# Kernel tuning notes

Hardware: AMD Instinct MI355X
Metric: run time of the kernel (lower is better)

## Reference

```python
import jax, jax.numpy as jnp
import numpy as np

T, BLOCK, SIG = 4096, 1024, 1024
LAM = 0.25


def _lstm_cell(x, h, c, Wih, Whh, bih, bhh):
    # PyTorch LSTM gate order: i, f, g, o
    gates = x @ Wih.T + h @ Whh.T + bih + bhh  # [1, 4H]
    i, f, g, o = jnp.split(gates, 4, axis=-1)
    i = jax.nn.sigmoid(i)
    f = jax.nn.sigmoid(f)
    g = jnp.tanh(g)
    o = jax.nn.sigmoid(o)
    c_new = f * c + i * g
    h_new = o * jnp.tanh(c_new)
    return h_new, c_new


def setup_inputs() -> dict:
    key = jax.random.key(0)
    ks = jax.random.split(key, 9)
    ke = 1.0 / np.sqrt(SIG)
    kd = 1.0 / np.sqrt(BLOCK)
    inputs = jax.random.normal(ks[0], (T, 1, BLOCK), dtype=jnp.float32)
    enc_Wih = jax.random.uniform(ks[1], (4 * SIG, BLOCK), jnp.float32, -ke, ke)
    enc_Whh = jax.random.uniform(ks[2], (4 * SIG, SIG), jnp.float32, -ke, ke)
    enc_bih = jax.random.uniform(ks[3], (4 * SIG,), jnp.float32, -ke, ke)
    enc_bhh = jax.random.uniform(ks[4], (4 * SIG,), jnp.float32, -ke, ke)
    dec_Wih = jax.random.uniform(ks[5], (4 * BLOCK, SIG), jnp.float32, -kd, kd)
    dec_Whh = jax.random.uniform(ks[6], (4 * BLOCK, BLOCK), jnp.float32, -kd, kd)
    dec_bih = jax.random.uniform(ks[7], (4 * BLOCK,), jnp.float32, -kd, kd)
    dec_bhh = jax.random.uniform(ks[8], (4 * BLOCK,), jnp.float32, -kd, kd)
    return {"inputs": inputs, "enc_Wih": enc_Wih, "enc_Whh": enc_Whh,
            "enc_bih": enc_bih, "enc_bhh": enc_bhh, "dec_Wih": dec_Wih,
            "dec_Whh": dec_Whh, "dec_bih": dec_bih, "dec_bhh": dec_bhh}


def reference(inputs, enc_Wih, enc_Whh, enc_bih, enc_bhh,
              dec_Wih, dec_Whh, dec_bih, dec_bhh):
    H = enc_Whh.shape[1]
    B = inputs.shape[-1]

    # encode: full-sequence LSTM, zero initial state, batch=1
    def enc_step(carry, x):
        h, c = carry
        h, c = _lstm_cell(x, h, c, enc_Wih, enc_Whh, enc_bih, enc_bhh)
        return (h, c), h

    h0 = jnp.zeros((1, H), inputs.dtype)
    c0 = jnp.zeros((1, H), inputs.dtype)
    _, signal = jax.lax.scan(enc_step, (h0, c0), inputs)  # [T, 1, H]

    # decode: one LSTM step per i; h0 reset to inputs[i], cell state carried
    def dec_step(c, xs):
        x, h_init = xs  # x = signal[i+1], h_init = inputs[i]
        h, c = _lstm_cell(x, h_init, c, dec_Wih, dec_Whh, dec_bih, dec_bhh)
        return c, h

    cdec0 = jnp.zeros((1, B), inputs.dtype)
    _, decoded = jax.lax.scan(dec_step, cdec0, (signal[1:], inputs[:-1]))  # [T-1, 1, B]

    target = inputs[1:]
    mse_loss = jnp.mean((decoded - target) ** 2)
    l1_reg = jnp.sum(jnp.abs(signal)) / signal.size
    loss = mse_loss + LAM * l1_reg
    return loss, mse_loss, l1_reg
```

## Files before the change

kernel.cpp:

```cpp
#include <hip/hip_runtime.h>
#include <math.h>

#define TSTEPS 4096
#define DIM 1024
#define GDIM 4096
#define ENC_NB 64
#define NSEG 64
#define SEGLEN 64

typedef short bf16x8 __attribute__((ext_vector_type(8)));
typedef float f32x4 __attribute__((ext_vector_type(4)));
typedef unsigned int uint4v __attribute__((ext_vector_type(4)));

__device__ __forceinline__ float sigmoidf_(float x) {
    return 1.0f / (1.0f + expf(-x));
}

__device__ __forceinline__ void loadcvt(const float* __restrict__ p,
                                        bf16x8& hi, bf16x8& lo)
{
    float4 a = *(const float4*)p;
    float4 b = *(const float4*)(p + 4);
    float f[8] = {a.x, a.y, a.z, a.w, b.x, b.y, b.z, b.w};
    uint4v hw, lw;
    #pragma unroll
    for (int j = 0; j < 4; ++j) {
        unsigned u0 = __float_as_uint(f[2*j]);
        unsigned u1 = __float_as_uint(f[2*j+1]);
        unsigned m0 = u0 & 0xffff0000u;
        unsigned m1 = u1 & 0xffff0000u;
        float r0 = f[2*j]   - __uint_as_float(m0);
        float r1 = f[2*j+1] - __uint_as_float(m1);
        hw[j] = __builtin_amdgcn_perm(u1, u0, 0x07060302u);
        lw[j] = __builtin_amdgcn_perm(__float_as_uint(r1), __float_as_uint(r0),
                                      0x07060302u);
    }
    hi = __builtin_bit_cast(bf16x8, hw);
    lo = __builtin_bit_cast(bf16x8, lw);
}

template<bool DUAL>
__global__ __launch_bounds__(256)
void gemm_split(const float* __restrict__ A1, const float* __restrict__ B1,
                const float* __restrict__ A2, const float* __restrict__ B2,
                const float* __restrict__ bias1, const float* __restrict__ bias2,
                float* __restrict__ C, int N)
{
    const int lane = threadIdx.x & 63;
    const int wid  = threadIdx.x >> 6;
    const int m0 = blockIdx.y * 128 + (wid >> 1) * 64;
    const int n0 = blockIdx.x * 128 + (wid & 1) * 64;
    const int rA   = m0 + (lane & 15);
    const int cB   = n0 + (lane & 15);
    const int koff = (lane >> 4) * 8;

    f32x4 acc[4][4] = {};

    const int npass = DUAL ? 2 : 1;
    for (int pass = 0; pass < npass; ++pass) {
        const float* __restrict__ A = (DUAL && pass) ? A2 : A1;
        const float* __restrict__ B = (DUAL && pass) ? B2 : B1;
        for (int k0 = 0; k0 < 1024; k0 += 32) {
            bf16x8 ah[4], al[4], bh[4], bl[4];
            #pragma unroll
            for (int i = 0; i < 4; ++i)
                loadcvt(A + (size_t)(rA + i * 16) * 1024 + k0 + koff, ah[i], al[i]);
            #pragma unroll
            for (int j = 0; j < 4; ++j)
                loadcvt(B + (size_t)(cB + j * 16) * 1024 + k0 + koff, bh[j], bl[j]);
            #pragma unroll
            for (int i = 0; i < 4; ++i)
                #pragma unroll
                for (int j = 0; j < 4; ++j) {
                    acc[i][j] = __builtin_amdgcn_mfma_f32_16x16x32_bf16(
                        ah[i], bh[j], acc[i][j], 0, 0, 0);
                    acc[i][j] = __builtin_amdgcn_mfma_f32_16x16x32_bf16(
                        ah[i], bl[j], acc[i][j], 0, 0, 0);
                    acc[i][j] = __builtin_amdgcn_mfma_f32_16x16x32_bf16(
                        al[i], bh[j], acc[i][j], 0, 0, 0);
                }
        }
    }

    const int er = (lane >> 4) * 4;
    const int ec = lane & 15;
    #pragma unroll
    for (int j = 0; j < 4; ++j) {
        int col = n0 + j * 16 + ec;
        float bb = bias1[col] + bias2[col];
        #pragma unroll
        for (int i = 0; i < 4; ++i) {
            int rowb = m0 + i * 16 + er;
            #pragma unroll
            for (int r = 0; r < 4; ++r)
                C[(size_t)(rowb + r) * N + col] = acc[i][j][r] + bb;
        }
    }
}

__global__ __launch_bounds__(1024)
void encoder_scan(const float* __restrict__ Xg,
                  const float* __restrict__ Whh,
                  float* __restrict__ signal,
                  unsigned long long* __restrict__ slots)
{
    const int b = blockIdx.x;
    const int t = threadIdx.x;
    const int hbase = b * 16;
    const int r = t >> 4, sub = t & 15;
    const int q = r >> 4, hi = r & 15;
    const int grow = q * 1024 + hbase + hi;

    float4 w[16];
    {
        const float4* wrow = (const float4*)(Whh + (size_t)grow * 1024 + sub * 64);
        #pragma unroll
        for (int i = 0; i < 16; ++i) w[i] = wrow[i];
    }

    __shared__ float hls[16 * 68];
    __shared__ float gl[4][16];
    __shared__ float cs[16];
    if (t < 16) cs[t] = 0.f;
    __syncthreads();

    for (int step = 0; step < TSTEPS; ++step) {
        float xg = 0.f;
        if (sub == 0) xg = Xg[(size_t)step * GDIM + grow];

        unsigned long long v;
        {
            const unsigned long long* sp = slots + (size_t)(step & 1) * 1024 + t;
            while (true) {
                v = __hip_atomic_load(sp, __ATOMIC_RELAXED, __HIP_MEMORY_SCOPE_AGENT);
                if ((unsigned)(v >> 32) >= (unsigned)step) break;
                __builtin_amdgcn_s_sleep(1);
            }
        }
        hls[(t >> 6) * 68 + (t & 63)] = __uint_as_float((unsigned)v);
        __syncthreads();

        float s = 0.f;
        const float* hv = hls + sub * 68;
        #pragma unroll
        for (int i = 0; i < 16; ++i) {
            float4 h4 = *(const float4*)(hv + i * 4);
            s = fmaf(w[i].x, h4.x, s); s = fmaf(w[i].y, h4.y, s);
            s = fmaf(w[i].z, h4.z, s); s = fmaf(w[i].w, h4.w, s);
        }
        s += __shfl_xor(s, 1);
        s += __shfl_xor(s, 2);
        s += __shfl_xor(s, 4);
        s += __shfl_xor(s, 8);
        if (sub == 0) gl[q][hi] = s + xg;
        __syncthreads();

        if (t < 16) {
            float iv = sigmoidf_(gl[0][t]);
            float fv = sigmoidf_(gl[1][t]);
            float gv = tanhf(gl[2][t]);
            float ov = sigmoidf_(gl[3][t]);
            float c = fmaf(fv, cs[t], iv * gv);
            cs[t] = c;
            float h = ov * tanhf(c);
            signal[(size_t)step * DIM + hbase + t] = h;
            unsigned long long pv =
                ((unsigned long long)(unsigned)(step + 1) << 32) | __float_as_uint(h);
            __hip_atomic_store(slots + (size_t)((step + 1) & 1) * 1024 + hbase + t,
                               pv, __ATOMIC_RELAXED, __HIP_MEMORY_SCOPE_AGENT);
        }
    }
}

__global__ __launch_bounds__(256)
void dec_compose(const float* __restrict__ G, float* __restrict__ Aseg,
                 float* __restrict__ Bseg)
{
    const int j = blockIdx.x * 256 + threadIdx.x;
    const int s = blockIdx.y;
    const int t0 = s * SEGLEN;
    const int t1 = min(t0 + SEGLEN, TSTEPS - 1);
    float A = 1.f, Bv = 0.f;
    for (int t = t0; t < t1; ++t) {
        const float* g = G + (size_t)t * GDIM;
        float iv = sigmoidf_(g[j]);
        float fv = sigmoidf_(g[j + 1024]);
        float gv = tanhf(g[j + 2048]);
        A *= fv;
        Bv = fmaf(fv, Bv, iv * gv);
    }
    Aseg[s * DIM + j] = A;
    Bseg[s * DIM + j] = Bv;
}

__global__ __launch_bounds__(1024)
void dec_scan(const float* __restrict__ Aseg, const float* __restrict__ Bseg,
              float* __restrict__ cinit)
{
    const int j = threadIdx.x;
    float c = 0.f;
    for (int s = 0; s < NSEG; ++s) {
        cinit[s * DIM + j] = c;
        c = fmaf(Aseg[s * DIM + j], c, Bseg[s * DIM + j]);
    }
}

__global__ __launch_bounds__(256)
void dec_emit(const float* __restrict__ G, const float* __restrict__ inp,
              const float* __restrict__ cinit, float* __restrict__ mse_acc)
{
    const int j = blockIdx.x * 256 + threadIdx.x;
    const int s = blockIdx.y;
    const int t0 = s * SEGLEN;
    const int t1 = min(t0 + SEGLEN, TSTEPS - 1);
    float c = cinit[s * DIM + j];
    float acc = 0.f;
    for (int t = t0; t < t1; ++t) {
        const float* g = G + (size_t)t * GDIM;
        float iv = sigmoidf_(g[j]);
        float fv = sigmoidf_(g[j + 1024]);
        float gv = tanhf(g[j + 2048]);
        float ov = sigmoidf_(g[j + 3072]);
        c = fmaf(fv, c, iv * gv);
        float d = ov * tanhf(c);
        float diff = d - inp[(size_t)(t + 1) * DIM + j];
        acc = fmaf(diff, diff, acc);
    }
    #pragma unroll
    for (int off = 32; off >= 1; off >>= 1) acc += __shfl_xor(acc, off);
    if ((threadIdx.x & 63) == 0) atomicAdd(mse_acc, acc);
}

__global__ __launch_bounds__(256)
void l1_reduce(const float* __restrict__ x, float* __restrict__ acc)
{
    const size_t n4 = (size_t)TSTEPS * DIM / 4;
    size_t tid = (size_t)blockIdx.x * 256 + threadIdx.x;
    size_t stride = (size_t)gridDim.x * 256;
    float s = 0.f;
    for (size_t i = tid; i < n4; i += stride) {
        float4 v = ((const float4*)x)[i];
        s += fabsf(v.x) + fabsf(v.y) + fabsf(v.z) + fabsf(v.w);
    }
    #pragma unroll
    for (int off = 32; off >= 1; off >>= 1) s += __shfl_xor(s, off);
    if ((threadIdx.x & 63) == 0) atomicAdd(acc, s);
}

__global__ void finalize(const float* __restrict__ scal, float* __restrict__ out)
{
    float mse = scal[0] / ((float)(TSTEPS - 1) * (float)DIM);
    float l1  = scal[1] / ((float)TSTEPS * (float)DIM);
    out[0] = mse + 0.25f * l1;
    out[1] = mse;
    out[2] = l1;
}

extern "C" void kernel_launch(void* const* d_in, const int* in_sizes, int n_in,
                              void* d_out, int out_size, void* d_ws, size_t ws_size,
                              hipStream_t stream)
{
    const float* inputs  = (const float*)d_in[0];
    const float* enc_Wih = (const float*)d_in[1];
    const float* enc_Whh = (const float*)d_in[2];
    const float* enc_bih = (const float*)d_in[3];
    const float* enc_bhh = (const float*)d_in[4];
    const float* dec_Wih = (const float*)d_in[5];
    const float* dec_Whh = (const float*)d_in[6];
    const float* dec_bih = (const float*)d_in[7];
    const float* dec_bhh = (const float*)d_in[8];
    float* out = (float*)d_out;

    float* ws = (float*)d_ws;
    float* gates  = ws;
    float* signal = ws + (size_t)16777216;
    unsigned long long* slots =
        (unsigned long long*)(ws + (size_t)20972544);
    float* scal   = ws + (size_t)20976640;
    float* Aseg   = ws + (size_t)20976648;
    float* Bseg   = ws + (size_t)21042184;
    float* cinit  = ws + (size_t)21107720;
    float* mse_acc = scal + 0;
    float* l1_acc  = scal + 1;

    hipMemsetAsync(ws + (size_t)20971520, 0, (size_t)(1024 + 4096 + 8) * 4, stream);

    dim3 b256(256);
    gemm_split<false><<<dim3(32, 32), b256, 0, stream>>>(
        inputs, enc_Wih, nullptr, nullptr, enc_bih, enc_bhh, gates, GDIM);
    encoder_scan<<<dim3(ENC_NB), dim3(1024), 0, stream>>>(
        gates, enc_Whh, signal, slots);
    gemm_split<true><<<dim3(32, 32), b256, 0, stream>>>(
        signal + DIM, dec_Wih, inputs, dec_Whh, dec_bih, dec_bhh, gates, GDIM);
    dec_compose<<<dim3(4, NSEG), b256, 0, stream>>>(gates, Aseg, Bseg);
    dec_scan<<<dim3(1), dim3(1024), 0, stream>>>(Aseg, Bseg, cinit);
    dec_emit<<<dim3(4, NSEG), b256, 0, stream>>>(gates, inputs, cinit, mse_acc);
    l1_reduce<<<dim3(256), b256, 0, stream>>>(signal, l1_acc);
    finalize<<<dim3(1), dim3(1), 0, stream>>>(scal, out);
}
```

Measured before the change: 9.082 ms.

## Restructure encoder scan per-wavefront, drop syncthreads, fuse L1 reduction

Each of the 16 wavefronts in a block now owns one hidden unit's four gate rows. The gate activations are exchanged with wave shuffles instead of shared memory, which removes the second __syncthreads per timestep and the single-thread cell update. The h staging buffer is double-buffered, and the spin-wait issues several pipelined atomic loads without sleeping, to cut cross-block sync latency on the serial critical path. The L1 sum is accumulated inside the encoder and the separate l1_reduce kernel is removed, at the cost of busier polling and a float atomicAdd per wavefront.

```diff
diff --git a/kernel.cpp b/kernel.cpp
--- a/kernel.cpp
+++ b/kernel.cpp
@@ -102,74 +102,83 @@
 void encoder_scan(const float* __restrict__ Xg,
                   const float* __restrict__ Whh,
                   float* __restrict__ signal,
-                  unsigned long long* __restrict__ slots)
+                  unsigned long long* __restrict__ slots,
+                  float* __restrict__ l1_acc)
 {
     const int b = blockIdx.x;
     const int t = threadIdx.x;
     const int hbase = b * 16;
-    const int r = t >> 4, sub = t & 15;
-    const int q = r >> 4, hi = r & 15;
-    const int grow = q * 1024 + hbase + hi;
-
-    float4 w[16];
+    const int w = t >> 6;
+    const int j = t & 63;
+    const int q = j >> 4;
+    const int sub = j & 15;
+    const int ch = hbase + w;
+    const int grow = q * 1024 + ch;
+
+    float4 wreg[16];
     {
         const float4* wrow = (const float4*)(Whh + (size_t)grow * 1024 + sub * 64);
         #pragma unroll
-        for (int i = 0; i < 16; ++i) w[i] = wrow[i];
-    }
-
-    __shared__ float hls[16 * 68];
-    __shared__ float gl[4][16];
-    __shared__ float cs[16];
-    if (t < 16) cs[t] = 0.f;
-    __syncthreads();
+        for (int i = 0; i < 16; ++i) wreg[i] = wrow[i];
+    }
+
+    __shared__ float hls[2][16 * 68];
+
+    float c = 0.f;
+    float l1 = 0.f;
 
     for (int step = 0; step < TSTEPS; ++step) {
+        const unsigned us = (unsigned)step;
         float xg = 0.f;
         if (sub == 0) xg = Xg[(size_t)step * GDIM + grow];
 
-        unsigned long long v;
-        {
-            const unsigned long long* sp = slots + (size_t)(step & 1) * 1024 + t;
-            while (true) {
-                v = __hip_atomic_load(sp, __ATOMIC_RELAXED, __HIP_MEMORY_SCOPE_AGENT);
-                if ((unsigned)(v >> 32) >= (unsigned)step) break;
-                __builtin_amdgcn_s_sleep(1);
-            }
-        }
-        hls[(t >> 6) * 68 + (t & 63)] = __uint_as_float((unsigned)v);
+        const unsigned long long* sp = slots + (size_t)(step & 1) * 1024 + t;
+        unsigned long long v  = __hip_atomic_load(sp, __ATOMIC_RELAXED, __HIP_MEMORY_SCOPE_AGENT);
+        unsigned long long v1 = __hip_atomic_load(sp, __ATOMIC_RELAXED, __HIP_MEMORY_SCOPE_AGENT);
+        unsigned long long v2 = __hip_atomic_load(sp, __ATOMIC_RELAXED, __HIP_MEMORY_SCOPE_AGENT);
+        while ((unsigned)(v >> 32) < us) {
+            v = v1; v1 = v2;
+            v2 = __hip_atomic_load(sp, __ATOMIC_RELAXED, __HIP_MEMORY_SCOPE_AGENT);
+        }
+
+        float* hb = hls[step & 1];
+        hb[w * 68 + j] = __uint_as_float((unsigned)v);
         __syncthreads();
 
         float s = 0.f;
-        const float* hv = hls + sub * 68;
+        const float* hv = hb + sub * 68;
         #pragma unroll
         for (int i = 0; i < 16; ++i) {
             float4 h4 = *(const float4*)(hv + i * 4);
-            s = fmaf(w[i].x, h4.x, s); s = fmaf(w[i].y, h4.y, s);
-            s = fmaf(w[i].z, h4.z, s); s = fmaf(w[i].w, h4.w, s);
+            s = fmaf(wreg[i].x, h4.x, s); s = fmaf(wreg[i].y, h4.y, s);
+            s = fmaf(wreg[i].z, h4.z, s); s = fmaf(wreg[i].w, h4.w, s);
         }
         s += __shfl_xor(s, 1);
         s += __shfl_xor(s, 2);
         s += __shfl_xor(s, 4);
         s += __shfl_xor(s, 8);
-        if (sub == 0) gl[q][hi] = s + xg;
-        __syncthreads();
-
-        if (t < 16) {
-            float iv = sigmoidf_(gl[0][t]);
-            float fv = sigmoidf_(gl[1][t]);
-            float gv = tanhf(gl[2][t]);
-            float ov = sigmoidf_(gl[3][t]);
-            float c = fmaf(fv, cs[t], iv * gv);
-            cs[t] = c;
+
+        float act = 0.f;
+        if (sub == 0) {
+            float pre = s + xg;
+            act = (q == 2) ? tanhf(pre) : sigmoidf_(pre);
+        }
+        float fv = __shfl(act, 16);
+        float gv = __shfl(act, 32);
+        float ov = __shfl(act, 48);
+        if (j == 0) {
+            float iv = act;
+            c = fmaf(fv, c, iv * gv);
             float h = ov * tanhf(c);
-            signal[(size_t)step * DIM + hbase + t] = h;
             unsigned long long pv =
-                ((unsigned long long)(unsigned)(step + 1) << 32) | __float_as_uint(h);
-            __hip_atomic_store(slots + (size_t)((step + 1) & 1) * 1024 + hbase + t,
+                ((unsigned long long)(us + 1) << 32) | __float_as_uint(h);
+            __hip_atomic_store(slots + (size_t)((step + 1) & 1) * 1024 + ch,
                                pv, __ATOMIC_RELAXED, __HIP_MEMORY_SCOPE_AGENT);
-        }
-    }
+            signal[(size_t)step * DIM + ch] = h;
+            l1 += fabsf(h);
+        }
+    }
+    if (j == 0) atomicAdd(l1_acc, l1);
 }
 
 __global__ __launch_bounds__(256)
@@ -231,22 +240,6 @@
     if ((threadIdx.x & 63) == 0) atomicAdd(mse_acc, acc);
 }
 
-__global__ __launch_bounds__(256)
-void l1_reduce(const float* __restrict__ x, float* __restrict__ acc)
-{
-    const size_t n4 = (size_t)TSTEPS * DIM / 4;
-    size_t tid = (size_t)blockIdx.x * 256 + threadIdx.x;
-    size_t stride = (size_t)gridDim.x * 256;
-    float s = 0.f;
-    for (size_t i = tid; i < n4; i += stride) {
-        float4 v = ((const float4*)x)[i];
-        s += fabsf(v.x) + fabsf(v.y) + fabsf(v.z) + fabsf(v.w);
-    }
-    #pragma unroll
-    for (int off = 32; off >= 1; off >>= 1) s += __shfl_xor(s, off);
-    if ((threadIdx.x & 63) == 0) atomicAdd(acc, s);
-}
-
 __global__ void finalize(const float* __restrict__ scal, float* __restrict__ out)
 {
     float mse = scal[0] / ((float)(TSTEPS - 1) * (float)DIM);
@@ -289,12 +282,11 @@
     gemm_split<false><<<dim3(32, 32), b256, 0, stream>>>(
         inputs, enc_Wih, nullptr, nullptr, enc_bih, enc_bhh, gates, GDIM);
     encoder_scan<<<dim3(ENC_NB), dim3(1024), 0, stream>>>(
-        gates, enc_Whh, signal, slots);
+        gates, enc_Whh, signal, slots, l1_acc);
     gemm_split<true><<<dim3(32, 32), b256, 0, stream>>>(
         signal + DIM, dec_Wih, inputs, dec_Whh, dec_bih, dec_bhh, gates, GDIM);
     dec_compose<<<dim3(4, NSEG), b256, 0, stream>>>(gates, Aseg, Bseg);
     dec_scan<<<dim3(1), dim3(1024), 0, stream>>>(Aseg, Bseg, cinit);
     dec_emit<<<dim3(4, NSEG), b256, 0, stream>>>(gates, inputs, cinit, mse_acc);
-    l1_reduce<<<dim3(256), b256, 0, stream>>>(signal, l1_acc);
     finalize<<<dim3(1), dim3(1), 0, stream>>>(scal, out);
 }
```

Result: slower. 22.54 ms (+148.1%).
